# Performance work log

Measured on AMD Instinct MI355X. Metric: run time of the kernel, lower is better.

## Reference

```python
import jax, jax.numpy as jnp
import numpy as np

NUM_NODES = 50000
NUM_EDGES = 800000
NUM_GRAPHS = 256
FEAT = 128
STATE = 64
ROUNDS = 4
M = 32


def setup_inputs() -> dict:
    key = jax.random.key(0)
    ks = jax.random.split(key, 12)
    x = jax.random.normal(ks[0], (NUM_NODES, FEAT), dtype=jnp.float32)
    edge_index = jax.random.randint(ks[1], (2, NUM_EDGES), 0, NUM_NODES, dtype=jnp.int64)
    batch = jnp.sort(jax.random.randint(ks[2], (NUM_NODES,), 0, NUM_GRAPHS, dtype=jnp.int64))
    s = 0.1  # weight init scale
    return {
        "x": x,
        "edge_index": edge_index,
        "batch": batch,
        "in_W": jax.random.normal(ks[3], (FEAT, STATE), dtype=jnp.float32) * s,
        "in_b": jnp.zeros((STATE,), dtype=jnp.float32),
        "msg_W": jax.random.normal(ks[4], (ROUNDS, STATE, STATE), dtype=jnp.float32) * s,
        "msg_b": jnp.zeros((ROUNDS, STATE), dtype=jnp.float32),
        "upd_W": jax.random.normal(ks[5], (ROUNDS, STATE, STATE), dtype=jnp.float32) * s,
        "upd_b": jnp.zeros((ROUNDS, STATE), dtype=jnp.float32),
        "mean_W": jax.random.normal(ks[6], (STATE, M), dtype=jnp.float32) * s,
        "mean_b": jnp.zeros((M,), dtype=jnp.float32),
        "logvar_W": jax.random.normal(ks[7], (STATE, M), dtype=jnp.float32) * s,
        "logvar_b": jnp.zeros((M,), dtype=jnp.float32),
    }


def reference(x, edge_index, batch, in_W, in_b, msg_W, msg_b, upd_W, upd_b,
              mean_W, mean_b, logvar_W, logvar_b):
    num_nodes = x.shape[0]
    src, dst = edge_index[0], edge_index[1]  # (to, from) -> gather src, scatter dst
    # input net (dropout is identity in eval mode)
    state = jax.nn.relu(x @ in_W + in_b)  # [N, S]
    for r in range(ROUNDS):
        message = jax.nn.relu(state @ msg_W[r] + msg_b[r])          # [N, S]
        gathered = message[src]                                       # [E, S] irregular gather
        aggregated = jax.ops.segment_sum(gathered, dst, num_segments=num_nodes)  # [N, S] scatter-add
        state = state + jax.nn.relu(aggregated @ upd_W[r] + upd_b[r])
    graph_state = jax.ops.segment_sum(state, batch, num_segments=NUM_GRAPHS)  # [G, S]
    mean = graph_state @ mean_W + mean_b                              # [G, M]
    log_var = jnp.clip(graph_state @ logvar_W + logvar_b, -20.0, 2.0)
    std = jnp.exp(0.5 * log_var)
    return jnp.stack([mean, std])  # [2, G, M] -> Normal(mean, std) params
```

## Files before the change

### kernel.cpp

```cpp
#include <hip/hip_runtime.h>
#include <math.h>

#define NODES  50000
#define EDGES  800000
#define GRAPHS 256
#define FEAT   128
#define STATE  64
#define M_OUT  32
#define ROUNDS 4
#define NT32   ((NODES + 31) / 32)
#define HALF   32
#define PLANE  (50000L * 32L)
#define CAP    64
#define OVFMAX 8192

typedef unsigned short bfraw;

__device__ __forceinline__ float bf2f(bfraw u) {
    union { unsigned int i; float f; } v; v.i = ((unsigned int)u) << 16; return v.f;
}
__device__ __forceinline__ bfraw f2bf(float f) {
    union { float f; unsigned int i; } v; v.f = f;
    unsigned int r = v.i + 0x7FFF + ((v.i >> 16) & 1);
    return (bfraw)(r >> 16);
}
__device__ __forceinline__ int packbf(float lo, float hi) {
    return ((int)f2bf(hi) << 16) | (int)f2bf(lo);
}
__device__ __forceinline__ void addv8(float* acc, int4 v, float m) {
    union { int i; float f; } t;
    t.i = v.x << 16;                  acc[0] += t.f * m;
    t.i = v.x & (int)0xffff0000;      acc[1] += t.f * m;
    t.i = v.y << 16;                  acc[2] += t.f * m;
    t.i = v.y & (int)0xffff0000;      acc[3] += t.f * m;
    t.i = v.z << 16;                  acc[4] += t.f * m;
    t.i = v.z & (int)0xffff0000;      acc[5] += t.f * m;
    t.i = v.w << 16;                  acc[6] += t.f * m;
    t.i = v.w & (int)0xffff0000;      acc[7] += t.f * m;
}
__device__ __forceinline__ void unpack8(float* d, int4 v) {
    union { int i; float f; } t;
    t.i = v.x << 16;              d[0] = t.f;
    t.i = v.x & (int)0xffff0000;  d[1] = t.f;
    t.i = v.y << 16;              d[2] = t.f;
    t.i = v.y & (int)0xffff0000;  d[3] = t.f;
    t.i = v.z << 16;              d[4] = t.f;
    t.i = v.z & (int)0xffff0000;  d[5] = t.f;
    t.i = v.w << 16;              d[6] = t.f;
    t.i = v.w & (int)0xffff0000;  d[7] = t.f;
}
__device__ __forceinline__ int4 pack8(const float* a) {
    int4 o;
    o.x = packbf(a[0], a[1]); o.y = packbf(a[2], a[3]);
    o.z = packbf(a[4], a[5]); o.w = packbf(a[6], a[7]);
    return o;
}

__global__ __launch_bounds__(256) void k_gather(
    const int* __restrict__ cnt, const unsigned short* __restrict__ csr,
    const int* __restrict__ ovfc, const int* __restrict__ ovf,
    const bfraw* __restrict__ plane0, const bfraw* __restrict__ plane1,
    bfraw* __restrict__ aggH0, bfraw* __restrict__ aggH1)
{
    float dummy = 0.f;
    {
        const bfraw* p = (threadIdx.x < 128) ? plane0 : plane1;
        long s = (long)blockIdx.x * 1024 + (long)(threadIdx.x & 127) * 8;
        if (s + 8 <= PLANE) {
            int4 a = *(const int4*)(p + s);
            union { int i; float f; } t; t.i = a.x << 16;
            dummy = t.f;
        }
    }

    int n = blockIdx.x * 32 + (threadIdx.x >> 3);
    if (n >= NODES) return;
    const int q = (threadIdx.x & 7) * 8;
    const bfraw* plane = (q < HALF) ? plane0 : plane1;
    const int qq = (q < HALF) ? q : q - HALF;
    int cn = cnt[n]; if (cn > CAP) cn = CAP;
    int beg = n * CAP, end = beg + cn;

    float acc[8] = {0.f, 0.f, 0.f, 0.f, 0.f, 0.f, 0.f, 0.f};
    for (int i = beg; i < end; i += 8) {
        int last = end - 1;
        int i1 = i + 1 < last ? i + 1 : last;
        int i2 = i + 2 < last ? i + 2 : last;
        int i3 = i + 3 < last ? i + 3 : last;
        int i4 = i + 4 < last ? i + 4 : last;
        int i5 = i + 5 < last ? i + 5 : last;
        int i6 = i + 6 < last ? i + 6 : last;
        int i7 = i + 7 < last ? i + 7 : last;
        int s0 = csr[i],  s1 = csr[i1], s2 = csr[i2], s3 = csr[i3];
        int s4 = csr[i4], s5 = csr[i5], s6 = csr[i6], s7 = csr[i7];
        int4 v0 = *(const int4*)(plane + (long)s0 * HALF + qq);
        int4 v1 = *(const int4*)(plane + (long)s1 * HALF + qq);
        int4 v2 = *(const int4*)(plane + (long)s2 * HALF + qq);
        int4 v3 = *(const int4*)(plane + (long)s3 * HALF + qq);
        int4 v4 = *(const int4*)(plane + (long)s4 * HALF + qq);
        int4 v5 = *(const int4*)(plane + (long)s5 * HALF + qq);
        int4 v6 = *(const int4*)(plane + (long)s6 * HALF + qq);
        int4 v7 = *(const int4*)(plane + (long)s7 * HALF + qq);
        float m1 = (i + 1 < end) ? 1.f : 0.f;
        float m2 = (i + 2 < end) ? 1.f : 0.f;
        float m3 = (i + 3 < end) ? 1.f : 0.f;
        float m4 = (i + 4 < end) ? 1.f : 0.f;
        float m5 = (i + 5 < end) ? 1.f : 0.f;
        float m6 = (i + 6 < end) ? 1.f : 0.f;
        float m7 = (i + 7 < end) ? 1.f : 0.f;
        addv8(acc, v0, 1.f); addv8(acc, v1, m1);
        addv8(acc, v2, m2);  addv8(acc, v3, m3);
        addv8(acc, v4, m4);  addv8(acc, v5, m5);
        addv8(acc, v6, m6);  addv8(acc, v7, m7);
    }
    acc[0] += dummy * 0.0f;

    int oc = *ovfc;
    if (oc > 0) {
        if (oc > OVFMAX) oc = OVFMAX;
        for (int t = 0; t < oc; t++) {
            int pk = ovf[t];
            if ((pk >> 16) == n) {
                int4 v = *(const int4*)(plane + (long)(pk & 0xffff) * HALF + qq);
                addv8(acc, v, 1.f);
            }
        }
    }

    bfraw* aout = (q < HALF) ? (aggH0 + (long)n * HALF + qq) : (aggH1 + (long)n * HALF + qq);
    *(int4*)aout = pack8(acc);
}

__global__ __launch_bounds__(256) void k_in_msg(
    const int* __restrict__ ei, int* __restrict__ cnt,
    unsigned short* __restrict__ csr, int* __restrict__ ovfc, int* __restrict__ ovf,
    const float* __restrict__ x, const float* __restrict__ inW, const float* __restrict__ inb,
    const float* __restrict__ msgW, const float* __restrict__ msgb,
    float* __restrict__ state, bfraw* __restrict__ msg0, bfraw* __restrict__ msg1)
{
    __shared__ float sW[64 * STATE];
    __shared__ float sInb[STATE], sMsgb[STATE];
    __shared__ float sx[32 * 132];
    __shared__ float ss[32 * 68];

    const int e0 = blockIdx.x * 256 + threadIdx.x;
    const int e1 = e0 + NT32 * 256;
    const bool v1 = (e1 < EDGES);
    int src0 = __builtin_nontemporal_load(ei + e0);
    int dst0 = __builtin_nontemporal_load(ei + EDGES + e0);
    int src1 = 0, dst1 = 0;
    if (v1) {
        src1 = __builtin_nontemporal_load(ei + e1);
        dst1 = __builtin_nontemporal_load(ei + EDGES + e1);
    }

    const int row = threadIdx.x >> 3;
    const int q8  = (threadIdx.x & 7) << 3;
    const int base = blockIdx.x * 32;
    const int n = base + row;

    if (threadIdx.x < STATE) {
        sInb[threadIdx.x]  = inb[threadIdx.x];
        sMsgb[threadIdx.x] = msgb[threadIdx.x];
    }
    for (int i = threadIdx.x; i < 1024; i += 256) {
        int r = i >> 5, q = (i & 31) << 2;
        float4 v = make_float4(0.f, 0.f, 0.f, 0.f);
        if (base + r < NODES) v = *(const float4*)(x + (long)(base + r) * FEAT + q);
        *(float4*)(sx + r * 132 + q) = v;
    }
    for (int i = threadIdx.x; i < 1024; i += 256)
        *(float4*)(sW + i * 4) = *(const float4*)(inW + i * 4);
    __syncthreads();

    {
        int sl0 = atomicAdd(&cnt[dst0], 1);
        int sl1 = v1 ? atomicAdd(&cnt[dst1], 1) : 0;
        if (sl0 < CAP) csr[(long)dst0 * CAP + sl0] = (unsigned short)src0;
        else { int o = atomicAdd(ovfc, 1); if (o < OVFMAX) ovf[o] = (dst0 << 16) | src0; }
        if (v1) {
            if (sl1 < CAP) csr[(long)dst1 * CAP + sl1] = (unsigned short)src1;
            else { int o = atomicAdd(ovfc, 1); if (o < OVFMAX) ovf[o] = (dst1 << 16) | src1; }
        }
    }

    float a[8];
    #pragma unroll
    for (int j = 0; j < 8; j++) a[j] = sInb[q8 + j];
    const float* xr = sx + row * 132;
    #pragma unroll 8
    for (int k = 0; k < 64; k++) {
        float xv = xr[k];
        float4 w0 = *(const float4*)(sW + k * STATE + q8);
        float4 w1 = *(const float4*)(sW + k * STATE + q8 + 4);
        a[0] += xv * w0.x; a[1] += xv * w0.y; a[2] += xv * w0.z; a[3] += xv * w0.w;
        a[4] += xv * w1.x; a[5] += xv * w1.y; a[6] += xv * w1.z; a[7] += xv * w1.w;
    }
    __syncthreads();
    for (int i = threadIdx.x; i < 1024; i += 256)
        *(float4*)(sW + i * 4) = *(const float4*)(inW + 64 * STATE + i * 4);
    __syncthreads();
    #pragma unroll 8
    for (int k = 0; k < 64; k++) {
        float xv = xr[64 + k];
        float4 w0 = *(const float4*)(sW + k * STATE + q8);
        float4 w1 = *(const float4*)(sW + k * STATE + q8 + 4);
        a[0] += xv * w0.x; a[1] += xv * w0.y; a[2] += xv * w0.z; a[3] += xv * w0.w;
        a[4] += xv * w1.x; a[5] += xv * w1.y; a[6] += xv * w1.z; a[7] += xv * w1.w;
    }
    #pragma unroll
    for (int j = 0; j < 8; j++) a[j] = fmaxf(a[j], 0.f);
    if (n < NODES) {
        *(float4*)(state + (long)n * STATE + q8)     = make_float4(a[0], a[1], a[2], a[3]);
        *(float4*)(state + (long)n * STATE + q8 + 4) = make_float4(a[4], a[5], a[6], a[7]);
    }
    *(float4*)(ss + row * 68 + q8)     = make_float4(a[0], a[1], a[2], a[3]);
    *(float4*)(ss + row * 68 + q8 + 4) = make_float4(a[4], a[5], a[6], a[7]);
    __syncthreads();
    for (int i = threadIdx.x; i < 1024; i += 256)
        *(float4*)(sW + i * 4) = *(const float4*)(msgW + i * 4);
    __syncthreads();

    float m[8];
    #pragma unroll
    for (int j = 0; j < 8; j++) m[j] = sMsgb[q8 + j];
    const float* sr = ss + row * 68;
    #pragma unroll 8
    for (int k = 0; k < STATE; k++) {
        float sv = sr[k];
        float4 w0 = *(const float4*)(sW + k * STATE + q8);
        float4 w1 = *(const float4*)(sW + k * STATE + q8 + 4);
        m[0] += sv * w0.x; m[1] += sv * w0.y; m[2] += sv * w0.z; m[3] += sv * w0.w;
        m[4] += sv * w1.x; m[5] += sv * w1.y; m[6] += sv * w1.z; m[7] += sv * w1.w;
    }
    #pragma unroll
    for (int j = 0; j < 8; j++) m[j] = fmaxf(m[j], 0.f);
    if (n < NODES) {
        bfraw* dst = (q8 < HALF) ? (msg0 + (long)n * HALF + q8) : (msg1 + (long)n * HALF + (q8 - HALF));
        *(int4*)dst = pack8(m);
    }
}

__global__ __launch_bounds__(256) void k_upd_msg(
    const float* __restrict__ updW, const float* __restrict__ updb,
    const float* __restrict__ msgW, const float* __restrict__ msgb,
    const bfraw* __restrict__ aggH0, const bfraw* __restrict__ aggH1,
    float* __restrict__ state, bfraw* __restrict__ msg0, bfraw* __restrict__ msg1)
{
    __shared__ float sW[64 * STATE];
    __shared__ float sUpdb[STATE], sMsgb[STATE];
    __shared__ float sa[32 * 68], ss[32 * 68];

    const int row = threadIdx.x >> 3;
    const int q8  = (threadIdx.x & 7) << 3;
    const int base = blockIdx.x * 32;
    const int n = base + row;

    if (threadIdx.x < STATE) {
        sUpdb[threadIdx.x] = updb[threadIdx.x];
        sMsgb[threadIdx.x] = msgb[threadIdx.x];
    }
    for (int i = threadIdx.x; i < 1024; i += 256)
        *(float4*)(sW + i * 4) = *(const float4*)(updW + i * 4);
    {
        float tmp[8] = {0.f,0.f,0.f,0.f,0.f,0.f,0.f,0.f};
        if (n < NODES) {
            const bfraw* src = (q8 < HALF) ? (aggH0 + (long)n * HALF + q8)
                                           : (aggH1 + (long)n * HALF + (q8 - HALF));
            unpack8(tmp, *(const int4*)src);
        }
        *(float4*)(sa + row * 68 + q8)     = make_float4(tmp[0], tmp[1], tmp[2], tmp[3]);
        *(float4*)(sa + row * 68 + q8 + 4) = make_float4(tmp[4], tmp[5], tmp[6], tmp[7]);
    }
    __syncthreads();

    float a[8];
    #pragma unroll
    for (int j = 0; j < 8; j++) a[j] = sUpdb[q8 + j];
    const float* ar = sa + row * 68;
    #pragma unroll 8
    for (int k = 0; k < STATE; k++) {
        float av = ar[k];
        float4 w0 = *(const float4*)(sW + k * STATE + q8);
        float4 w1 = *(const float4*)(sW + k * STATE + q8 + 4);
        a[0] += av * w0.x; a[1] += av * w0.y; a[2] += av * w0.z; a[3] += av * w0.w;
        a[4] += av * w1.x; a[5] += av * w1.y; a[6] += av * w1.z; a[7] += av * w1.w;
    }
    #pragma unroll
    for (int j = 0; j < 8; j++) a[j] = fmaxf(a[j], 0.f);
    float s[8] = {0.f,0.f,0.f,0.f,0.f,0.f,0.f,0.f};
    if (n < NODES) {
        float4 st0 = *(const float4*)(state + (long)n * STATE + q8);
        float4 st1 = *(const float4*)(state + (long)n * STATE + q8 + 4);
        s[0] = st0.x + a[0]; s[1] = st0.y + a[1]; s[2] = st0.z + a[2]; s[3] = st0.w + a[3];
        s[4] = st1.x + a[4]; s[5] = st1.y + a[5]; s[6] = st1.z + a[6]; s[7] = st1.w + a[7];
        *(float4*)(state + (long)n * STATE + q8)     = make_float4(s[0], s[1], s[2], s[3]);
        *(float4*)(state + (long)n * STATE + q8 + 4) = make_float4(s[4], s[5], s[6], s[7]);
    }
    *(float4*)(ss + row * 68 + q8)     = make_float4(s[0], s[1], s[2], s[3]);
    *(float4*)(ss + row * 68 + q8 + 4) = make_float4(s[4], s[5], s[6], s[7]);
    __syncthreads();
    for (int i = threadIdx.x; i < 1024; i += 256)
        *(float4*)(sW + i * 4) = *(const float4*)(msgW + i * 4);
    __syncthreads();

    float m[8];
    #pragma unroll
    for (int j = 0; j < 8; j++) m[j] = sMsgb[q8 + j];
    const float* sr = ss + row * 68;
    #pragma unroll 8
    for (int k = 0; k < STATE; k++) {
        float sv = sr[k];
        float4 w0 = *(const float4*)(sW + k * STATE + q8);
        float4 w1 = *(const float4*)(sW + k * STATE + q8 + 4);
        m[0] += sv * w0.x; m[1] += sv * w0.y; m[2] += sv * w0.z; m[3] += sv * w0.w;
        m[4] += sv * w1.x; m[5] += sv * w1.y; m[6] += sv * w1.z; m[7] += sv * w1.w;
    }
    #pragma unroll
    for (int j = 0; j < 8; j++) m[j] = fmaxf(m[j], 0.f);
    if (n < NODES) {
        bfraw* dst = (q8 < HALF) ? (msg0 + (long)n * HALF + q8) : (msg1 + (long)n * HALF + (q8 - HALF));
        *(int4*)dst = pack8(m);
    }
}

__global__ __launch_bounds__(256) void k_upd_pool(
    const float* __restrict__ updW, const float* __restrict__ updb,
    const bfraw* __restrict__ aggH0, const bfraw* __restrict__ aggH1,
    const float* __restrict__ state, const int* __restrict__ batch,
    float* __restrict__ gs)
{
    __shared__ float sW[64 * STATE];
    __shared__ float sUpdb[STATE];
    __shared__ float sa[32 * 68];
    __shared__ float ssum[32 * 68];
    __shared__ int   sg[32];

    const int row = threadIdx.x >> 3;
    const int q8  = (threadIdx.x & 7) << 3;
    const int base = blockIdx.x * 32;
    const int n = base + row;

    if (threadIdx.x < STATE) sUpdb[threadIdx.x] = updb[threadIdx.x];
    for (int i = threadIdx.x; i < 1024; i += 256)
        *(float4*)(sW + i * 4) = *(const float4*)(updW + i * 4);
    {
        float tmp[8] = {0.f,0.f,0.f,0.f,0.f,0.f,0.f,0.f};
        if (n < NODES) {
            const bfraw* src = (q8 < HALF) ? (aggH0 + (long)n * HALF + q8)
                                           : (aggH1 + (long)n * HALF + (q8 - HALF));
            unpack8(tmp, *(const int4*)src);
        }
        *(float4*)(sa + row * 68 + q8)     = make_float4(tmp[0], tmp[1], tmp[2], tmp[3]);
        *(float4*)(sa + row * 68 + q8 + 4) = make_float4(tmp[4], tmp[5], tmp[6], tmp[7]);
    }
    if (threadIdx.x < 32) {
        int nn = base + threadIdx.x;
        sg[threadIdx.x] = batch[nn < NODES ? nn : NODES - 1];
    }
    __syncthreads();

    float a[8];
    #pragma unroll
    for (int j = 0; j < 8; j++) a[j] = sUpdb[q8 + j];
    const float* ar = sa + row * 68;
    #pragma unroll 8
    for (int k = 0; k < STATE; k++) {
        float av = ar[k];
        float4 w0 = *(const float4*)(sW + k * STATE + q8);
        float4 w1 = *(const float4*)(sW + k * STATE + q8 + 4);
        a[0] += av * w0.x; a[1] += av * w0.y; a[2] += av * w0.z; a[3] += av * w0.w;
        a[4] += av * w1.x; a[5] += av * w1.y; a[6] += av * w1.z; a[7] += av * w1.w;
    }
    float s[8] = {0.f,0.f,0.f,0.f,0.f,0.f,0.f,0.f};
    if (n < NODES) {
        float4 st0 = *(const float4*)(state + (long)n * STATE + q8);
        float4 st1 = *(const float4*)(state + (long)n * STATE + q8 + 4);
        s[0] = st0.x + fmaxf(a[0], 0.f); s[1] = st0.y + fmaxf(a[1], 0.f);
        s[2] = st0.z + fmaxf(a[2], 0.f); s[3] = st0.w + fmaxf(a[3], 0.f);
        s[4] = st1.x + fmaxf(a[4], 0.f); s[5] = st1.y + fmaxf(a[5], 0.f);
        s[6] = st1.z + fmaxf(a[6], 0.f); s[7] = st1.w + fmaxf(a[7], 0.f);
    }
    *(float4*)(ssum + row * 68 + q8)     = make_float4(s[0], s[1], s[2], s[3]);
    *(float4*)(ssum + row * 68 + q8 + 4) = make_float4(s[4], s[5], s[6], s[7]);
    __syncthreads();

    if (threadIdx.x < STATE) {
        const int f = threadIdx.x;
        float run = ssum[f];
        int g = sg[0];
        #pragma unroll
        for (int r = 1; r < 32; r++) {
            int g2 = sg[r];
            float v = ssum[r * 68 + f];
            if (g2 != g) {
                atomicAdd(&gs[g * STATE + f], run);
                run = v; g = g2;
            } else {
                run += v;
            }
        }
        atomicAdd(&gs[g * STATE + f], run);
    }
}

__global__ __launch_bounds__(64) void k_final(
    const float* __restrict__ gs,
    const float* __restrict__ meanW, const float* __restrict__ meanb,
    const float* __restrict__ lvW, const float* __restrict__ lvb,
    float* __restrict__ out)
{
    __shared__ float row[STATE];
    const int g = blockIdx.x;
    const int j = threadIdx.x;
    row[j] = gs[g * STATE + j];
    __syncthreads();
    if (j < M_OUT) {
        float acc = meanb[j];
        #pragma unroll
        for (int k = 0; k < STATE; k++) acc += row[k] * meanW[k * M_OUT + j];
        out[g * M_OUT + j] = acc;
    } else {
        int jj = j - M_OUT;
        float acc = lvb[jj];
        #pragma unroll
        for (int k = 0; k < STATE; k++) acc += row[k] * lvW[k * M_OUT + jj];
        acc = fminf(fmaxf(acc, -20.f), 2.f);
        out[GRAPHS * M_OUT + g * M_OUT + jj] = expf(0.5f * acc);
    }
}

extern "C" void kernel_launch(void* const* d_in, const int* in_sizes, int n_in,
                              void* d_out, int out_size, void* d_ws, size_t ws_size,
                              hipStream_t stream) {
    const float* x     = (const float*)d_in[0];
    const int*   ei    = (const int*)d_in[1];
    const int*   batch = (const int*)d_in[2];
    const float* inW   = (const float*)d_in[3];
    const float* inb   = (const float*)d_in[4];
    const float* msgW  = (const float*)d_in[5];
    const float* msgb  = (const float*)d_in[6];
    const float* updW  = (const float*)d_in[7];
    const float* updb  = (const float*)d_in[8];
    const float* meanW = (const float*)d_in[9];
    const float* meanb = (const float*)d_in[10];
    const float* lvW   = (const float*)d_in[11];
    const float* lvb   = (const float*)d_in[12];
    float* out = (float*)d_out;

    const size_t NS   = (size_t)NODES * STATE * sizeof(float);
    const size_t PLB  = (size_t)PLANE * sizeof(bfraw);
    const size_t AGH  = (size_t)NODES * HALF * sizeof(bfraw);
    char* ws = (char*)d_ws;
    size_t off = 0;
    auto alloc = [&](size_t bytes) { void* p = ws + off; off += (bytes + 255) & ~(size_t)255; return p; };
    float* state  = (float*)alloc(NS);
    bfraw* msgA0  = (bfraw*)alloc(PLB);
    bfraw* msgA1  = (bfraw*)alloc(PLB);
    bfraw* msgB0  = (bfraw*)alloc(PLB);
    bfraw* msgB1  = (bfraw*)alloc(PLB);
    bfraw* aggH0  = (bfraw*)alloc(AGH);
    bfraw* aggH1  = (bfraw*)alloc(AGH);
    float* gs     = (float*)alloc((size_t)GRAPHS * STATE * sizeof(float));
    int*   cnt    = (int*)alloc((size_t)NODES * sizeof(int));
    int*   ovfc   = (int*)alloc(256);
    int*   ovf    = (int*)alloc((size_t)OVFMAX * sizeof(int));
    unsigned short* csr = (unsigned short*)alloc((size_t)NODES * CAP * sizeof(unsigned short));

    hipMemsetAsync(cnt, 0, (size_t)NODES * sizeof(int), stream);
    hipMemsetAsync(ovfc, 0, sizeof(int), stream);
    hipMemsetAsync(gs, 0, (size_t)GRAPHS * STATE * sizeof(float), stream);

    k_in_msg<<<NT32, 256, 0, stream>>>(ei, cnt, csr, ovfc, ovf,
                                       x, inW, inb, msgW, msgb, state, msgA0, msgA1);

    bfraw *mi0 = msgA0, *mi1 = msgA1, *mo0 = msgB0, *mo1 = msgB1;
    for (int r = 0; r < ROUNDS; r++) {
        k_gather<<<NT32, 256, 0, stream>>>(cnt, csr, ovfc, ovf, mi0, mi1, aggH0, aggH1);
        if (r < ROUNDS - 1) {
            k_upd_msg<<<NT32, 256, 0, stream>>>(
                updW + r * STATE * STATE, updb + r * STATE,
                msgW + (r + 1) * STATE * STATE, msgb + (r + 1) * STATE,
                aggH0, aggH1, state, mo0, mo1);
            bfraw* t0 = mi0; mi0 = mo0; mo0 = t0;
            bfraw* t1 = mi1; mi1 = mo1; mo1 = t1;
        } else {
            k_upd_pool<<<NT32, 256, 0, stream>>>(
                updW + r * STATE * STATE, updb + r * STATE,
                aggH0, aggH1, state, batch, gs);
        }
    }

    k_final<<<GRAPHS, 64, 0, stream>>>(gs, meanW, meanb, lvW, lvb, out);
}
```

Before: 334.3 us.

## Fuse neighbor gather into update kernels and move CSR build after matmuls

The separate gather kernel is folded into the per-round update kernels: each block gathers its 32 nodes' neighbor messages straight into LDS in fp32, so the bf16 aggregate buffers and their global round trip disappear, along with four kernel launches. LDS is reused (sa serves for both aggregate and state) to cut shared memory, which adds an extra barrier. In k_in_msg the CSR-building atomics are moved after the matmul work, so their latency may overlap the compute. The fused kernels hold more registers and LDS during the gather, which may reduce occupancy for the latency-bound gather phase.

After: 308.7 us. 1.08x faster.

```diff
diff --git a/kernel.cpp b/kernel.cpp
--- a/kernel.cpp
+++ b/kernel.cpp
@@ -38,17 +38,6 @@
     t.i = v.w << 16;                  acc[6] += t.f * m;
     t.i = v.w & (int)0xffff0000;      acc[7] += t.f * m;
 }
-__device__ __forceinline__ void unpack8(float* d, int4 v) {
-    union { int i; float f; } t;
-    t.i = v.x << 16;              d[0] = t.f;
-    t.i = v.x & (int)0xffff0000;  d[1] = t.f;
-    t.i = v.y << 16;              d[2] = t.f;
-    t.i = v.y & (int)0xffff0000;  d[3] = t.f;
-    t.i = v.z << 16;              d[4] = t.f;
-    t.i = v.z & (int)0xffff0000;  d[5] = t.f;
-    t.i = v.w << 16;              d[6] = t.f;
-    t.i = v.w & (int)0xffff0000;  d[7] = t.f;
-}
 __device__ __forceinline__ int4 pack8(const float* a) {
     int4 o;
     o.x = packbf(a[0], a[1]); o.y = packbf(a[2], a[3]);
@@ -56,11 +45,11 @@
     return o;
 }
 
-__global__ __launch_bounds__(256) void k_gather(
+__device__ __forceinline__ void gather_to_lds(
     const int* __restrict__ cnt, const unsigned short* __restrict__ csr,
     const int* __restrict__ ovfc, const int* __restrict__ ovf,
     const bfraw* __restrict__ plane0, const bfraw* __restrict__ plane1,
-    bfraw* __restrict__ aggH0, bfraw* __restrict__ aggH1)
+    float* __restrict__ sa)
 {
     float dummy = 0.f;
     {
@@ -73,12 +62,14 @@
         }
     }
 
-    int n = blockIdx.x * 32 + (threadIdx.x >> 3);
-    if (n >= NODES) return;
-    const int q = (threadIdx.x & 7) * 8;
+    const int row = threadIdx.x >> 3;
+    const int q   = (threadIdx.x & 7) * 8;
+    const int n   = blockIdx.x * 32 + row;
     const bfraw* plane = (q < HALF) ? plane0 : plane1;
     const int qq = (q < HALF) ? q : q - HALF;
-    int cn = cnt[n]; if (cn > CAP) cn = CAP;
+
+    int cn = (n < NODES) ? cnt[n] : 0;
+    if (cn > CAP) cn = CAP;
     int beg = n * CAP, end = beg + cn;
 
     float acc[8] = {0.f, 0.f, 0.f, 0.f, 0.f, 0.f, 0.f, 0.f};
@@ -127,8 +118,8 @@
         }
     }
 
-    bfraw* aout = (q < HALF) ? (aggH0 + (long)n * HALF + qq) : (aggH1 + (long)n * HALF + qq);
-    *(int4*)aout = pack8(acc);
+    *(float4*)(sa + row * 68 + q)     = make_float4(acc[0], acc[1], acc[2], acc[3]);
+    *(float4*)(sa + row * 68 + q + 4) = make_float4(acc[4], acc[5], acc[6], acc[7]);
 }
 
 __global__ __launch_bounds__(256) void k_in_msg(
@@ -173,6 +164,62 @@
         *(float4*)(sW + i * 4) = *(const float4*)(inW + i * 4);
     __syncthreads();
 
+    float a[8];
+    #pragma unroll
+    for (int j = 0; j < 8; j++) a[j] = sInb[q8 + j];
+    const float* xr = sx + row * 132;
+    #pragma unroll 8
+    for (int k = 0; k < 64; k++) {
+        float xv = xr[k];
+        float4 w0 = *(const float4*)(sW + k * STATE + q8);
+        float4 w1 = *(const float4*)(sW + k * STATE + q8 + 4);
+        a[0] += xv * w0.x; a[1] += xv * w0.y; a[2] += xv * w0.z; a[3] += xv * w0.w;
+        a[4] += xv * w1.x; a[5] += xv * w1.y; a[6] += xv * w1.z; a[7] += xv * w1.w;
+    }
+    __syncthreads();
+    for (int i = threadIdx.x; i < 1024; i += 256)
+        *(float4*)(sW + i * 4) = *(const float4*)(inW + 64 * STATE + i * 4);
+    __syncthreads();
+    #pragma unroll 8
+    for (int k = 0; k < 64; k++) {
+        float xv = xr[64 + k];
+        float4 w0 = *(const float4*)(sW + k * STATE + q8);
+        float4 w1 = *(const float4*)(sW + k * STATE + q8 + 4);
+        a[0] += xv * w0.x; a[1] += xv * w0.y; a[2] += xv * w0.z; a[3] += xv * w0.w;
+        a[4] += xv * w1.x; a[5] += xv * w1.y; a[6] += xv * w1.z; a[7] += xv * w1.w;
+    }
+    #pragma unroll
+    for (int j = 0; j < 8; j++) a[j] = fmaxf(a[j], 0.f);
+    if (n < NODES) {
+        *(float4*)(state + (long)n * STATE + q8)     = make_float4(a[0], a[1], a[2], a[3]);
+        *(float4*)(state + (long)n * STATE + q8 + 4) = make_float4(a[4], a[5], a[6], a[7]);
+    }
+    *(float4*)(ss + row * 68 + q8)     = make_float4(a[0], a[1], a[2], a[3]);
+    *(float4*)(ss + row * 68 + q8 + 4) = make_float4(a[4], a[5], a[6], a[7]);
+    __syncthreads();
+    for (int i = threadIdx.x; i < 1024; i += 256)
+        *(float4*)(sW + i * 4) = *(const float4*)(msgW + i * 4);
+    __syncthreads();
+
+    float m[8];
+    #pragma unroll
+    for (int j = 0; j < 8; j++) m[j] = sMsgb[q8 + j];
+    const float* sr = ss + row * 68;
+    #pragma unroll 8
+    for (int k = 0; k < STATE; k++) {
+        float sv = sr[k];
+        float4 w0 = *(const float4*)(sW + k * STATE + q8);
+        float4 w1 = *(const float4*)(sW + k * STATE + q8 + 4);
+        m[0] += sv * w0.x; m[1] += sv * w0.y; m[2] += sv * w0.z; m[3] += sv * w0.w;
+        m[4] += sv * w1.x; m[5] += sv * w1.y; m[6] += sv * w1.z; m[7] += sv * w1.w;
+    }
+    #pragma unroll
+    for (int j = 0; j < 8; j++) m[j] = fmaxf(m[j], 0.f);
+    if (n < NODES) {
+        bfraw* dst = (q8 < HALF) ? (msg0 + (long)n * HALF + q8) : (msg1 + (long)n * HALF + (q8 - HALF));
+        *(int4*)dst = pack8(m);
+    }
+
     {
         int sl0 = atomicAdd(&cnt[dst0], 1);
         int sl1 = v1 ? atomicAdd(&cnt[dst1], 1) : 0;
@@ -183,78 +230,23 @@
             else { int o = atomicAdd(ovfc, 1); if (o < OVFMAX) ovf[o] = (dst1 << 16) | src1; }
         }
     }
-
-    float a[8];
-    #pragma unroll
-    for (int j = 0; j < 8; j++) a[j] = sInb[q8 + j];
-    const float* xr = sx + row * 132;
-    #pragma unroll 8
-    for (int k = 0; k < 64; k++) {
-        float xv = xr[k];
-        float4 w0 = *(const float4*)(sW + k * STATE + q8);
-        float4 w1 = *(const float4*)(sW + k * STATE + q8 + 4);
-        a[0] += xv * w0.x; a[1] += xv * w0.y; a[2] += xv * w0.z; a[3] += xv * w0.w;
-        a[4] += xv * w1.x; a[5] += xv * w1.y; a[6] += xv * w1.z; a[7] += xv * w1.w;
-    }
-    __syncthreads();
-    for (int i = threadIdx.x; i < 1024; i += 256)
-        *(float4*)(sW + i * 4) = *(const float4*)(inW + 64 * STATE + i * 4);
-    __syncthreads();
-    #pragma unroll 8
-    for (int k = 0; k < 64; k++) {
-        float xv = xr[64 + k];
-        float4 w0 = *(const float4*)(sW + k * STATE + q8);
-        float4 w1 = *(const float4*)(sW + k * STATE + q8 + 4);
-        a[0] += xv * w0.x; a[1] += xv * w0.y; a[2] += xv * w0.z; a[3] += xv * w0.w;
-        a[4] += xv * w1.x; a[5] += xv * w1.y; a[6] += xv * w1.z; a[7] += xv * w1.w;
-    }
-    #pragma unroll
-    for (int j = 0; j < 8; j++) a[j] = fmaxf(a[j], 0.f);
-    if (n < NODES) {
-        *(float4*)(state + (long)n * STATE + q8)     = make_float4(a[0], a[1], a[2], a[3]);
-        *(float4*)(state + (long)n * STATE + q8 + 4) = make_float4(a[4], a[5], a[6], a[7]);
-    }
-    *(float4*)(ss + row * 68 + q8)     = make_float4(a[0], a[1], a[2], a[3]);
-    *(float4*)(ss + row * 68 + q8 + 4) = make_float4(a[4], a[5], a[6], a[7]);
-    __syncthreads();
-    for (int i = threadIdx.x; i < 1024; i += 256)
-        *(float4*)(sW + i * 4) = *(const float4*)(msgW + i * 4);
-    __syncthreads();
-
-    float m[8];
-    #pragma unroll
-    for (int j = 0; j < 8; j++) m[j] = sMsgb[q8 + j];
-    const float* sr = ss + row * 68;
-    #pragma unroll 8
-    for (int k = 0; k < STATE; k++) {
-        float sv = sr[k];
-        float4 w0 = *(const float4*)(sW + k * STATE + q8);
-        float4 w1 = *(const float4*)(sW + k * STATE + q8 + 4);
-        m[0] += sv * w0.x; m[1] += sv * w0.y; m[2] += sv * w0.z; m[3] += sv * w0.w;
-        m[4] += sv * w1.x; m[5] += sv * w1.y; m[6] += sv * w1.z; m[7] += sv * w1.w;
-    }
-    #pragma unroll
-    for (int j = 0; j < 8; j++) m[j] = fmaxf(m[j], 0.f);
-    if (n < NODES) {
-        bfraw* dst = (q8 < HALF) ? (msg0 + (long)n * HALF + q8) : (msg1 + (long)n * HALF + (q8 - HALF));
-        *(int4*)dst = pack8(m);
-    }
-}
-
-__global__ __launch_bounds__(256) void k_upd_msg(
+}
+
+__global__ __launch_bounds__(256) void k_round_msg(
+    const int* __restrict__ cnt, const unsigned short* __restrict__ csr,
+    const int* __restrict__ ovfc, const int* __restrict__ ovf,
+    const bfraw* __restrict__ plane0, const bfraw* __restrict__ plane1,
     const float* __restrict__ updW, const float* __restrict__ updb,
     const float* __restrict__ msgW, const float* __restrict__ msgb,
-    const bfraw* __restrict__ aggH0, const bfraw* __restrict__ aggH1,
     float* __restrict__ state, bfraw* __restrict__ msg0, bfraw* __restrict__ msg1)
 {
     __shared__ float sW[64 * STATE];
     __shared__ float sUpdb[STATE], sMsgb[STATE];
-    __shared__ float sa[32 * 68], ss[32 * 68];
+    __shared__ float sa[32 * 68];
 
     const int row = threadIdx.x >> 3;
     const int q8  = (threadIdx.x & 7) << 3;
-    const int base = blockIdx.x * 32;
-    const int n = base + row;
+    const int n = blockIdx.x * 32 + row;
 
     if (threadIdx.x < STATE) {
         sUpdb[threadIdx.x] = updb[threadIdx.x];
@@ -262,16 +254,8 @@
     }
     for (int i = threadIdx.x; i < 1024; i += 256)
         *(float4*)(sW + i * 4) = *(const float4*)(updW + i * 4);
-    {
-        float tmp[8] = {0.f,0.f,0.f,0.f,0.f,0.f,0.f,0.f};
-        if (n < NODES) {
-            const bfraw* src = (q8 < HALF) ? (aggH0 + (long)n * HALF + q8)
-                                           : (aggH1 + (long)n * HALF + (q8 - HALF));
-            unpack8(tmp, *(const int4*)src);
-        }
-        *(float4*)(sa + row * 68 + q8)     = make_float4(tmp[0], tmp[1], tmp[2], tmp[3]);
-        *(float4*)(sa + row * 68 + q8 + 4) = make_float4(tmp[4], tmp[5], tmp[6], tmp[7]);
-    }
+
+    gather_to_lds(cnt, csr, ovfc, ovf, plane0, plane1, sa);
     __syncthreads();
 
     float a[8];
@@ -297,9 +281,9 @@
         *(float4*)(state + (long)n * STATE + q8)     = make_float4(s[0], s[1], s[2], s[3]);
         *(float4*)(state + (long)n * STATE + q8 + 4) = make_float4(s[4], s[5], s[6], s[7]);
     }
-    *(float4*)(ss + row * 68 + q8)     = make_float4(s[0], s[1], s[2], s[3]);
-    *(float4*)(ss + row * 68 + q8 + 4) = make_float4(s[4], s[5], s[6], s[7]);
-    __syncthreads();
+    __syncthreads();
+    *(float4*)(sa + row * 68 + q8)     = make_float4(s[0], s[1], s[2], s[3]);
+    *(float4*)(sa + row * 68 + q8 + 4) = make_float4(s[4], s[5], s[6], s[7]);
     for (int i = threadIdx.x; i < 1024; i += 256)
         *(float4*)(sW + i * 4) = *(const float4*)(msgW + i * 4);
     __syncthreads();
@@ -307,7 +291,7 @@
     float m[8];
     #pragma unroll
     for (int j = 0; j < 8; j++) m[j] = sMsgb[q8 + j];
-    const float* sr = ss + row * 68;
+    const float* sr = sa + row * 68;
     #pragma unroll 8
     for (int k = 0; k < STATE; k++) {
         float sv = sr[k];
@@ -324,16 +308,17 @@
     }
 }
 
-__global__ __launch_bounds__(256) void k_upd_pool(
+__global__ __launch_bounds__(256) void k_round_pool(
+    const int* __restrict__ cnt, const unsigned short* __restrict__ csr,
+    const int* __restrict__ ovfc, const int* __restrict__ ovf,
+    const bfraw* __restrict__ plane0, const bfraw* __restrict__ plane1,
     const float* __restrict__ updW, const float* __restrict__ updb,
-    const bfraw* __restrict__ aggH0, const bfraw* __restrict__ aggH1,
     const float* __restrict__ state, const int* __restrict__ batch,
     float* __restrict__ gs)
 {
     __shared__ float sW[64 * STATE];
     __shared__ float sUpdb[STATE];
     __shared__ float sa[32 * 68];
-    __shared__ float ssum[32 * 68];
     __shared__ int   sg[32];
 
     const int row = threadIdx.x >> 3;
@@ -344,20 +329,12 @@
     if (threadIdx.x < STATE) sUpdb[threadIdx.x] = updb[threadIdx.x];
     for (int i = threadIdx.x; i < 1024; i += 256)
         *(float4*)(sW + i * 4) = *(const float4*)(updW + i * 4);
-    {
-        float tmp[8] = {0.f,0.f,0.f,0.f,0.f,0.f,0.f,0.f};
-        if (n < NODES) {
-            const bfraw* src = (q8 < HALF) ? (aggH0 + (long)n * HALF + q8)
-                                           : (aggH1 + (long)n * HALF + (q8 - HALF));
-            unpack8(tmp, *(const int4*)src);
-        }
-        *(float4*)(sa + row * 68 + q8)     = make_float4(tmp[0], tmp[1], tmp[2], tmp[3]);
-        *(float4*)(sa + row * 68 + q8 + 4) = make_float4(tmp[4], tmp[5], tmp[6], tmp[7]);
-    }
     if (threadIdx.x < 32) {
         int nn = base + threadIdx.x;
         sg[threadIdx.x] = batch[nn < NODES ? nn : NODES - 1];
     }
+
+    gather_to_lds(cnt, csr, ovfc, ovf, plane0, plane1, sa);
     __syncthreads();
 
     float a[8];
@@ -381,18 +358,19 @@
         s[4] = st1.x + fmaxf(a[4], 0.f); s[5] = st1.y + fmaxf(a[5], 0.f);
         s[6] = st1.z + fmaxf(a[6], 0.f); s[7] = st1.w + fmaxf(a[7], 0.f);
     }
-    *(float4*)(ssum + row * 68 + q8)     = make_float4(s[0], s[1], s[2], s[3]);
-    *(float4*)(ssum + row * 68 + q8 + 4) = make_float4(s[4], s[5], s[6], s[7]);
+    __syncthreads();
+    *(float4*)(sa + row * 68 + q8)     = make_float4(s[0], s[1], s[2], s[3]);
+    *(float4*)(sa + row * 68 + q8 + 4) = make_float4(s[4], s[5], s[6], s[7]);
     __syncthreads();
 
     if (threadIdx.x < STATE) {
         const int f = threadIdx.x;
-        float run = ssum[f];
+        float run = sa[f];
         int g = sg[0];
         #pragma unroll
         for (int r = 1; r < 32; r++) {
             int g2 = sg[r];
-            float v = ssum[r * 68 + f];
+            float v = sa[r * 68 + f];
             if (g2 != g) {
                 atomicAdd(&gs[g * STATE + f], run);
                 run = v; g = g2;
@@ -450,7 +428,6 @@
 
     const size_t NS   = (size_t)NODES * STATE * sizeof(float);
     const size_t PLB  = (size_t)PLANE * sizeof(bfraw);
-    const size_t AGH  = (size_t)NODES * HALF * sizeof(bfraw);
     char* ws = (char*)d_ws;
     size_t off = 0;
     auto alloc = [&](size_t bytes) { void* p = ws + off; off += (bytes + 255) & ~(size_t)255; return p; };
@@ -459,8 +436,6 @@
     bfraw* msgA1  = (bfraw*)alloc(PLB);
     bfraw* msgB0  = (bfraw*)alloc(PLB);
     bfraw* msgB1  = (bfraw*)alloc(PLB);
-    bfraw* aggH0  = (bfraw*)alloc(AGH);
-    bfraw* aggH1  = (bfraw*)alloc(AGH);
     float* gs     = (float*)alloc((size_t)GRAPHS * STATE * sizeof(float));
     int*   cnt    = (int*)alloc((size_t)NODES * sizeof(int));
     int*   ovfc   = (int*)alloc(256);
@@ -476,18 +451,19 @@
 
     bfraw *mi0 = msgA0, *mi1 = msgA1, *mo0 = msgB0, *mo1 = msgB1;
     for (int r = 0; r < ROUNDS; r++) {
-        k_gather<<<NT32, 256, 0, stream>>>(cnt, csr, ovfc, ovf, mi0, mi1, aggH0, aggH1);
         if (r < ROUNDS - 1) {
-            k_upd_msg<<<NT32, 256, 0, stream>>>(
+            k_round_msg<<<NT32, 256, 0, stream>>>(
+                cnt, csr, ovfc, ovf, mi0, mi1,
                 updW + r * STATE * STATE, updb + r * STATE,
                 msgW + (r + 1) * STATE * STATE, msgb + (r + 1) * STATE,
-                aggH0, aggH1, state, mo0, mo1);
+                state, mo0, mo1);
             bfraw* t0 = mi0; mi0 = mo0; mo0 = t0;
             bfraw* t1 = mi1; mi1 = mo1; mo1 = t1;
         } else {
-            k_upd_pool<<<NT32, 256, 0, stream>>>(
+            k_round_pool<<<NT32, 256, 0, stream>>>(
+                cnt, csr, ovfc, ovf, mi0, mi1,
                 updW + r * STATE * STATE, updb + r * STATE,
-                aggH0, aggH1, state, batch, gs);
+                state, batch, gs);
         }
     }
 
```
